# Performance work log

Measured on AMD Instinct MI355X. Metric: run time of the kernel, lower is better.

## Reference

```python
import jax, jax.numpy as jnp
import numpy as np

B, N, DIM = 4, 2048, 1024
HEADS, DHEAD = 16, 64
INNER = HEADS * DHEAD  # 1024


def _sigma(t):
    # elu(x) + 1 feature map (strictly positive)
    return jax.nn.elu(t) + 1.0


def setup_inputs() -> dict:
    key = jax.random.key(0)
    k1, k2, k3, k4, k5 = jax.random.split(key, 5)
    x = jax.random.normal(k1, (B, N, DIM), dtype=jnp.float32)
    M = jax.random.normal(k2, (B, HEADS, DHEAD, DHEAD), dtype=jnp.float32)
    Z = jnp.ones((B, HEADS, DHEAD, 1), dtype=jnp.float32)
    W_qkv = jax.random.normal(k3, (DIM, 3 * INNER), dtype=jnp.float32) * (DIM ** -0.5)
    beta_lin = jnp.ones((1,), dtype=jnp.float32) * 4.6     # Linear_Attention.beta
    beta_gate = jax.random.normal(k4, (1, HEADS, 1, 1), dtype=jnp.float32)  # per-head gate
    return {"x": x, "M": M, "Z": Z, "W_qkv": W_qkv, "beta_lin": beta_lin, "beta_gate": beta_gate}


def reference(x, M, Z, W_qkv, beta_lin, beta_gate):
    b, n, _ = x.shape
    scale = DHEAD ** -0.5

    qkv = x @ W_qkv                                   # [b, n, 3*inner]
    q, k, v = jnp.split(qkv, 3, axis=-1)
    # b n (h d) -> b h n d
    to_heads = lambda t: t.reshape(b, n, HEADS, DHEAD).transpose(0, 2, 1, 3)
    q, k, v = to_heads(q), to_heads(k), to_heads(v)

    # ---- linear-attention compressive memory branch ----
    sq = _sigma(q)                                    # [b h n d]
    sk = _sigma(k)
    A_mem = jnp.einsum('bhnd,bhdv->bhnv', sq, M) / jnp.einsum('bhnd,bhdi->bhni', sq, Z)
    moment = jnp.einsum('bhnd,bhdv->bhnv', sk, M) / jnp.einsum('bhnd,bhdi->bhni', sk, Z)

    # EMA state update (training path)
    beta_m = jnp.clip(jax.nn.sigmoid(beta_lin), 0.9, 0.999)  # scalar in (0.9, 0.999)
    Z_new = beta_m * Z + jnp.sum(sk, axis=-2)[..., None]      # [b h d 1]
    M_new = beta_m * M + jnp.einsum('bhnd,bhnv->bhdv', sk, v - moment)

    # ---- standard dot-product attention branch ----
    dots = jnp.einsum('bhid,bhjd->bhij', q, k) * scale
    attn = jax.nn.softmax(dots, axis=-1)
    A_dot = jnp.einsum('bhij,bhjd->bhid', attn, v)

    # ---- learned per-head gate ----
    g = jax.nn.sigmoid(beta_gate)                     # [1 h 1 1]
    A = g * A_mem + (1.0 - g) * A_dot                 # [b h n d]
    A = A.transpose(0, 2, 1, 3).reshape(b, n, INNER)  # b h n d -> b n (h d)
    return (A, M_new, Z_new)
```

## Files before the change

### kernel.cpp

```cpp
#include <hip/hip_runtime.h>
#include <math.h>

#define B_ 4
#define N_ 2048
#define DIM_ 1024
#define H_ 16
#define D_ 64
#define INNER_ 1024
#define BH_ (B_*H_)

#define A_ELEMS  (B_*N_*INNER_)
#define M_ELEMS  (BH_*D_*D_)
#define Z_ELEMS  (BH_*D_)

#define SC_LOG2E 0.18033688011112042f

typedef __attribute__((ext_vector_type(8))) short short8;
typedef __attribute__((ext_vector_type(4))) float f32x4;
typedef __attribute__((ext_vector_type(4))) unsigned short us4;
typedef unsigned short u16;

typedef const unsigned int __attribute__((address_space(1))) gu32;
typedef unsigned int __attribute__((address_space(3))) su32;

__device__ __forceinline__ u16 f2bf(float f) {
    unsigned int u = __float_as_uint(f);
    u += 0x7fffu + ((u >> 16) & 1u);
    return (u16)(u >> 16);
}
__device__ __forceinline__ float bf2f(u16 s) {
    return __uint_as_float(((unsigned int)s) << 16);
}
__device__ __forceinline__ float sigma_f(float x) {
    return x > 0.f ? x + 1.f : __expf(x);
}
__device__ __forceinline__ short8 sig8(short8 in) {
    short8 out;
    u16* ip = (u16*)&in; u16* op = (u16*)&out;
    #pragma unroll
    for (int c = 0; c < 8; c++) op[c] = f2bf(sigma_f(bf2f(ip[c])));
    return out;
}

__global__ __launch_bounds__(256) void cvt_x(const float* __restrict__ x,
                                             u16* __restrict__ xb) {
    long i = ((long)blockIdx.x * 256 + threadIdx.x) * 4;
    float4 f = *(const float4*)&x[i];
    us4 o = {f2bf(f.x), f2bf(f.y), f2bf(f.z), f2bf(f.w)};
    *(us4*)&xb[i] = o;
}

__global__ __launch_bounds__(256) void cvt_w(const float* __restrict__ W,
                                             u16* __restrict__ Wt) {
    __shared__ u16 T[64 * 68];
    const int t  = threadIdx.x;
    const int n0 = blockIdx.x * 64, k0 = blockIdx.y * 64;
    #pragma unroll
    for (int i = 0; i < 4; i++) {
        int r  = (t >> 4) + i * 16;
        int c4 = (t & 15) * 4;
        float4 f = *(const float4*)&W[(long)(k0 + r) * 3072 + n0 + c4];
        T[(c4 + 0) * 68 + r] = f2bf(f.x);
        T[(c4 + 1) * 68 + r] = f2bf(f.y);
        T[(c4 + 2) * 68 + r] = f2bf(f.z);
        T[(c4 + 3) * 68 + r] = f2bf(f.w);
    }
    __syncthreads();
    #pragma unroll
    for (int i = 0; i < 4; i++) {
        int n  = (t >> 4) + i * 16;
        int k4 = (t & 15) * 4;
        us4 o;
        o.x = T[n * 68 + k4];     o.y = T[n * 68 + k4 + 1];
        o.z = T[n * 68 + k4 + 2]; o.w = T[n * 68 + k4 + 3];
        *(us4*)&Wt[(long)(n0 + n) * 1024 + k0 + k4] = o;
    }
}

__global__ __launch_bounds__(256) void qkv_mfma(
    const u16* __restrict__ xb, const u16* __restrict__ Wt,
    u16* __restrict__ q, u16* __restrict__ k, u16* __restrict__ v) {
    __shared__ u16 As[2][128 * 32];
    __shared__ u16 Bs[2][128 * 32];
    const int t = threadIdx.x, w = t >> 6, lane = t & 63;
    const int quad = lane >> 4, l16 = lane & 15;

    const int lin = blockIdx.x;
    const int wg  = (lin & 7) * 192 + (lin >> 3);
    const int j0  = (wg % 24) * 128;
    const int m0  = (wg / 24) * 128;
    const int mw = (w >> 1) * 64, nw = (w & 1) * 64;

    const int srow = t >> 2;
    const int scol = (t & 3) * 8;

    const u16* pa0 = xb + (long)(m0 + srow) * 1024 + scol;
    const u16* pa1 = pa0 + (long)64 * 1024;
    const u16* pb0 = Wt + (long)(j0 + srow) * 1024 + scol;
    const u16* pb1 = pb0 + (long)64 * 1024;
    su32* da0 = (su32*)&As[0][srow * 32 + scol];
    su32* da1 = (su32*)&As[0][(srow + 64) * 32 + scol];
    su32* db0 = (su32*)&Bs[0][srow * 32 + scol];
    su32* db1 = (su32*)&Bs[0][(srow + 64) * 32 + scol];
    const int half = 128 * 32 / 2;

    f32x4 acc[4][4] = {};

    __builtin_amdgcn_global_load_lds((gu32*)pa0, da0, 16, 0, 0);
    __builtin_amdgcn_global_load_lds((gu32*)pa1, da1, 16, 0, 0);
    __builtin_amdgcn_global_load_lds((gu32*)pb0, db0, 16, 0, 0);
    __builtin_amdgcn_global_load_lds((gu32*)pb1, db1, 16, 0, 0);
    pa0 += 32; pa1 += 32; pb0 += 32; pb1 += 32;
    __syncthreads();

    for (int kt = 0; kt < 32; ++kt) {
        const int cur = kt & 1;
        if (kt + 1 < 32) {
            const int nxs = (cur ^ 1) * half;
            __builtin_amdgcn_global_load_lds((gu32*)pa0, da0 + nxs, 16, 0, 0);
            __builtin_amdgcn_global_load_lds((gu32*)pa1, da1 + nxs, 16, 0, 0);
            __builtin_amdgcn_global_load_lds((gu32*)pb0, db0 + nxs, 16, 0, 0);
            __builtin_amdgcn_global_load_lds((gu32*)pb1, db1 + nxs, 16, 0, 0);
            pa0 += 32; pa1 += 32; pb0 += 32; pb1 += 32;
        }

        short8 af[4], bf[4];
        #pragma unroll
        for (int mt = 0; mt < 4; mt++)
            af[mt] = *(const short8*)&As[cur][(mw + mt * 16 + l16) * 32 + quad * 8];
        #pragma unroll
        for (int nt = 0; nt < 4; nt++)
            bf[nt] = *(const short8*)&Bs[cur][(nw + nt * 16 + l16) * 32 + quad * 8];
        #pragma unroll
        for (int mt = 0; mt < 4; mt++)
            #pragma unroll
            for (int nt = 0; nt < 4; nt++)
                acc[mt][nt] = __builtin_amdgcn_mfma_f32_16x16x32_bf16(
                    af[mt], bf[nt], acc[mt][nt], 0, 0, 0);

        __syncthreads();
    }

    const int cb0 = j0 + nw;
    const int which = cb0 >> 10;
    u16* dstsel = (which == 0) ? q : (which == 1) ? k : v;
    const int bq = (m0 + mw) >> 11;
    const int nb = (m0 + mw) & 2047;
    const int lanoff = quad * 256 + l16;
    #pragma unroll
    for (int nt = 0; nt < 4; nt++) {
        const int cb = cb0 + nt * 16;
        const int hh = (cb & 1023) >> 6;
        const int dc = cb & 63;
        u16* dstp = dstsel + ((long)(bq * H_ + hh) * N_ + nb) * D_ + dc;
        #pragma unroll
        for (int mt = 0; mt < 4; mt++)
            #pragma unroll
            for (int r = 0; r < 4; r++)
                dstp[(mt * 16 + r) * 64 + lanoff] = f2bf(acc[mt][nt][r]);
    }
}

__global__ __launch_bounds__(256) void vt_transpose(
    const u16* __restrict__ vb, u16* __restrict__ vT) {
    __shared__ u16 T[64 * 72];
    const int bh = blockIdx.y;
    const int n0 = blockIdx.x * 64;
    const int t  = threadIdx.x;
    const int jj = t >> 3, kg = (t & 7) * 8;
    #pragma unroll
    for (int i = 0; i < 2; i++) {
        int j = jj + i * 32;
        short8 vv = *(const short8*)&vb[(((long)bh * N_ + n0 + j) << 6) + kg];
        u16* vp = (u16*)&vv;
        int jc = j ^ kg;
        #pragma unroll
        for (int c = 0; c < 8; c++) T[(kg + c) * 72 + jc] = vp[c];
    }
    __syncthreads();
    const int d = t >> 2, sg = (t & 3) * 16, xr = d & 56;
    short8 a0 = *(const short8*)&T[d * 72 + (sg ^ xr)];
    short8 a1 = *(const short8*)&T[d * 72 + ((sg + 8) ^ xr)];
    u16* dst = vT + ((long)bh * 64 + d) * 2048 + n0 + sg;
    *(short8*)dst       = a0;
    *(short8*)(dst + 8) = a1;
}

__global__ __launch_bounds__(256) void init_mz(
    const float* __restrict__ M, const float* __restrict__ Z,
    const float* __restrict__ beta_lin,
    float* __restrict__ outM, float* __restrict__ outZ) {
    float beta = 1.f / (1.f + __expf(-beta_lin[0]));
    beta = fminf(fmaxf(beta, 0.9f), 0.999f);
    int i = blockIdx.x * 256 + threadIdx.x;
    if (i < M_ELEMS) outM[i] = beta * M[i];
    if (i < Z_ELEMS) outZ[i] = beta * Z[i];
}

__global__ __launch_bounds__(256) void linear_mfma(
    const u16* __restrict__ qg, const u16* __restrict__ kg_,
    const u16* __restrict__ vTg, const float* __restrict__ Mg,
    const float* __restrict__ Zg, const float* __restrict__ beta_gate,
    float* __restrict__ outA, float* __restrict__ outM, float* __restrict__ outZ) {
    __shared__ u16 MTz[80 * 72];
    __shared__ u16 sqsh[64 * 72];
    __shared__ u16 sksh[64 * 72];
    __shared__ u16 skT[64 * 72];
    __shared__ u16 vT[64 * 72];
    __shared__ u16 vmT[80 * 72];
    __shared__ float dks[64];

    const int bh = blockIdx.y, b = bh >> 4, h = bh & 15;
    const int t = threadIdx.x, w = t >> 6, lane = t & 63;
    const int quad = lane >> 4, l16 = lane & 15;
    const long bhN = (long)bh * N_;

    #pragma unroll
    for (int i = 0; i < 4; i++) {
        int d  = (t >> 4) + i * 16;
        int c4 = (t & 15) * 4;
        float4 f = *(const float4*)&Mg[bh * 4096 + d * 64 + c4];
        MTz[(c4 + 0) * 72 + d] = f2bf(f.x);
        MTz[(c4 + 1) * 72 + d] = f2bf(f.y);
        MTz[(c4 + 2) * 72 + d] = f2bf(f.z);
        MTz[(c4 + 3) * 72 + d] = f2bf(f.w);
    }
    if (t < 64) {
        MTz[64 * 72 + t] = f2bf(Zg[bh * 64 + t]);
        vmT[64 * 72 + t] = f2bf(1.0f);
    }
    for (int e = t; e < 15 * 72; e += 256) {
        MTz[65 * 72 + e] = 0;
        vmT[65 * 72 + e] = 0;
    }
    if (t >= 64 && t < 72) { MTz[64 * 72 + t] = 0; vmT[64 * 72 + t] = 0; }

    const float g = 1.f / (1.f + __expf(-beta_gate[h]));

    f32x4 macc[5] = {};

    const int jj = t >> 3;
    const int kgp = (t & 7) * 8;
    const int srow = t >> 2;
    const int sg   = (t & 3) * 16;

    for (int c0 = 0; c0 < 256; c0 += 64) {
        const int n0c = blockIdx.x * 256 + c0;
        __syncthreads();

        #pragma unroll
        for (int i = 0; i < 2; i++) {
            int j = jj + i * 32;
            long gb = ((bhN + n0c + j) << 6) + kgp;
            short8 q8 = sig8(*(const short8*)&qg[gb]);
            short8 k8 = sig8(*(const short8*)&kg_[gb]);
            *(short8*)&sqsh[j * 72 + kgp] = q8;
            *(short8*)&sksh[j * 72 + kgp] = k8;
            u16* kp = (u16*)&k8;
            int jc = j ^ kgp;
            #pragma unroll
            for (int c = 0; c < 8; c++) skT[(kgp + c) * 72 + jc] = kp[c];
        }
        {
            const u16* vp = vTg + ((long)bh * 64 + srow) * 2048 + n0c + sg;
            *(short8*)&vT[srow * 72 + sg]     = *(const short8*)vp;
            *(short8*)&vT[srow * 72 + sg + 8] = *(const short8*)(vp + 8);
        }
        __syncthreads();

        {
            short8 a0 = *(const short8*)&sqsh[(w * 16 + l16) * 72 + quad * 8];
            short8 a1 = *(const short8*)&sqsh[(w * 16 + l16) * 72 + 32 + quad * 8];
            f32x4 am[5];
            #pragma unroll
            for (int ct = 0; ct < 5; ct++) {
                short8 b0 = *(const short8*)&MTz[(ct * 16 + l16) * 72 + quad * 8];
                short8 b1 = *(const short8*)&MTz[(ct * 16 + l16) * 72 + 32 + quad * 8];
                f32x4 acc = {};
                acc = __builtin_amdgcn_mfma_f32_16x16x32_bf16(a0, b0, acc, 0, 0, 0);
                acc = __builtin_amdgcn_mfma_f32_16x16x32_bf16(a1, b1, acc, 0, 0, 0);
                am[ct] = acc;
            }
            #pragma unroll
            for (int r = 0; r < 4; r++) {
                float dq  = __shfl(am[4][r], lane & 48, 64);
                float inv = __builtin_amdgcn_rcpf(dq);
                int n = n0c + w * 16 + quad * 4 + r;
                long row = ((long)(b * N_ + n)) * INNER_ + h * 64;
                #pragma unroll
                for (int ct = 0; ct < 4; ct++)
                    outA[row + ct * 16 + l16] = g * am[ct][r] * inv;
            }
        }

        f32x4 mt_[4];
        {
            short8 a0 = *(const short8*)&MTz[(w * 16 + l16) * 72 + quad * 8];
            short8 a1 = *(const short8*)&MTz[(w * 16 + l16) * 72 + 32 + quad * 8];
            #pragma unroll
            for (int ct = 0; ct < 4; ct++) {
                short8 b0 = *(const short8*)&sksh[(ct * 16 + l16) * 72 + quad * 8];
                short8 b1 = *(const short8*)&sksh[(ct * 16 + l16) * 72 + 32 + quad * 8];
                f32x4 acc = {};
                acc = __builtin_amdgcn_mfma_f32_16x16x32_bf16(a0, b0, acc, 0, 0, 0);
                acc = __builtin_amdgcn_mfma_f32_16x16x32_bf16(a1, b1, acc, 0, 0, 0);
                mt_[ct] = acc;
            }
            short8 z0 = *(const short8*)&MTz[(64 + l16) * 72 + quad * 8];
            short8 z1 = *(const short8*)&MTz[(64 + l16) * 72 + 32 + quad * 8];
            short8 b0 = *(const short8*)&sksh[(w * 16 + l16) * 72 + quad * 8];
            short8 b1 = *(const short8*)&sksh[(w * 16 + l16) * 72 + 32 + quad * 8];
            f32x4 acc = {};
            acc = __builtin_amdgcn_mfma_f32_16x16x32_bf16(z0, b0, acc, 0, 0, 0);
            acc = __builtin_amdgcn_mfma_f32_16x16x32_bf16(z1, b1, acc, 0, 0, 0);
            if (quad == 0) dks[w * 16 + l16] = __builtin_amdgcn_rcpf(acc[0]);
        }
        __syncthreads();

        #pragma unroll
        for (int ct = 0; ct < 4; ct++) {
            float invdk = dks[ct * 16 + l16];
            #pragma unroll
            for (int r = 0; r < 4; r++) {
                int vd = w * 16 + quad * 4 + r;
                float vv = bf2f(vT[vd * 72 + ct * 16 + l16]);
                vmT[vd * 72 + ct * 16 + l16] = f2bf(vv - mt_[ct][r] * invdk);
            }
        }
        __syncthreads();

        {
            int drow = w * 16 + l16, xr = drow & 56;
            short8 a0 = *(const short8*)&skT[drow * 72 + ((quad * 8) ^ xr)];
            short8 a1 = *(const short8*)&skT[drow * 72 + ((32 + quad * 8) ^ xr)];
            #pragma unroll
            for (int ct = 0; ct < 5; ct++) {
                short8 b0 = *(const short8*)&vmT[(ct * 16 + l16) * 72 + quad * 8];
                short8 b1 = *(const short8*)&vmT[(ct * 16 + l16) * 72 + 32 + quad * 8];
                macc[ct] = __builtin_amdgcn_mfma_f32_16x16x32_bf16(a0, b0, macc[ct], 0, 0, 0);
                macc[ct] = __builtin_amdgcn_mfma_f32_16x16x32_bf16(a1, b1, macc[ct], 0, 0, 0);
            }
        }
    }

    #pragma unroll
    for (int ct = 0; ct < 4; ct++)
        #pragma unroll
        for (int r = 0; r < 4; r++) {
            int d = w * 16 + quad * 4 + r;
            atomicAdd(&outM[bh * 4096 + d * 64 + ct * 16 + l16], macc[ct][r]);
        }
    if (l16 == 0)
        #pragma unroll
        for (int r = 0; r < 4; r++)
            atomicAdd(&outZ[bh * 64 + w * 16 + quad * 4 + r], macc[4][r]);
}

__global__ __launch_bounds__(256, 2) void flash_mfma(
    const u16* __restrict__ qb, const u16* __restrict__ kb,
    const u16* __restrict__ vTg, const float* __restrict__ beta_gate,
    float* __restrict__ outA) {
    __shared__ u16 Ks[64 * 68];
    __shared__ u16 Vt[64 * 68];

    const int lin = blockIdx.x;
    const int wg  = (lin & 7) * 64 + (lin >> 3);
    const int bh  = wg >> 3;
    const int n0  = (wg & 7) * 256;
    const int b = bh >> 4, h = bh & 15;
    const int t = threadIdx.x, w = t >> 6, lane = t & 63;
    const int quad = lane >> 4, l16 = lane & 15;
    const long bhN = (long)bh * N_;

    const int srow = t >> 2;
    const int sg   = (t & 3) * 16;
    const int jloc = srow & 31;
    const int krow = (srow & 32) + ((jloc & 4) << 2) + ((jloc >> 3) << 2) + (jloc & 3);

    const u16* kbase  = kb + (bhN << 6);
    const u16* vtbase = vTg + (long)bh * 64 * 2048;

    short8 qf[4][2];
    #pragma unroll
    for (int mi = 0; mi < 4; mi++) {
        long qrow = bhN + n0 + w * 64 + mi * 16 + l16;
        qf[mi][0] = *(const short8*)&qb[(qrow << 6) + quad * 8];
        qf[mi][1] = *(const short8*)&qb[(qrow << 6) + 32 + quad * 8];
        #pragma unroll
        for (int z = 0; z < 2; z++) {
            u16* p = (u16*)&qf[mi][z];
            #pragma unroll
            for (int c = 0; c < 8; c++) p[c] = f2bf(bf2f(p[c]) * SC_LOG2E);
        }
    }

    const short8 onesf = {0x3F80, 0x3F80, 0x3F80, 0x3F80,
                          0x3F80, 0x3F80, 0x3F80, 0x3F80};

    short8 kr0, kr1, vr0, vr1;
    {
        const u16* kp = kbase + ((long)srow << 6) + sg;
        kr0 = *(const short8*)kp;
        kr1 = *(const short8*)(kp + 8);
        const u16* vp = vtbase + (long)srow * 2048 + sg;
        vr0 = *(const short8*)vp;
        vr1 = *(const short8*)(vp + 8);
    }

    f32x4 of[4][4] = {};
    f32x4 ol[4] = {};

    for (int j0 = 0; j0 < N_; j0 += 64) {
        __syncthreads();
        *(short8*)&Ks[krow * 68 + sg]     = kr0;
        *(short8*)&Ks[krow * 68 + sg + 8] = kr1;
        *(short8*)&Vt[srow * 68 + sg]     = vr0;
        *(short8*)&Vt[srow * 68 + sg + 8] = vr1;
        __syncthreads();

        if (j0 + 64 < N_) {
            const u16* kp = kbase + ((long)(j0 + 64 + srow) << 6) + sg;
            kr0 = *(const short8*)kp;
            kr1 = *(const short8*)(kp + 8);
            const u16* vp = vtbase + (long)srow * 2048 + j0 + 64 + sg;
            vr0 = *(const short8*)vp;
            vr1 = *(const short8*)(vp + 8);
        }

        #pragma unroll
        for (int g = 0; g < 2; g++) {
            const int rb = g * 32;
            short8 kA0 = *(const short8*)&Ks[(rb + l16) * 68 + quad * 8];
            short8 kA1 = *(const short8*)&Ks[(rb + l16) * 68 + 32 + quad * 8];
            short8 kB0 = *(const short8*)&Ks[(rb + 16 + l16) * 68 + quad * 8];
            short8 kB1 = *(const short8*)&Ks[(rb + 16 + l16) * 68 + 32 + quad * 8];
            short8 vf[4];
            #pragma unroll
            for (int nt = 0; nt < 4; nt++)
                vf[nt] = *(const short8*)&Vt[(nt * 16 + l16) * 68 + rb + quad * 8];

            #pragma unroll
            for (int mi = 0; mi < 4; mi++) {
                f32x4 st0 = {}, st1 = {};
                __builtin_amdgcn_s_setprio(1);
                st0 = __builtin_amdgcn_mfma_f32_16x16x32_bf16(kA0, qf[mi][0], st0, 0, 0, 0);
                st0 = __builtin_amdgcn_mfma_f32_16x16x32_bf16(kA1, qf[mi][1], st0, 0, 0, 0);
                st1 = __builtin_amdgcn_mfma_f32_16x16x32_bf16(kB0, qf[mi][0], st1, 0, 0, 0);
                st1 = __builtin_amdgcn_mfma_f32_16x16x32_bf16(kB1, qf[mi][1], st1, 0, 0, 0);
                __builtin_amdgcn_s_setprio(0);
                float p0 = __builtin_amdgcn_exp2f(st0[0]);
                float p1 = __builtin_amdgcn_exp2f(st0[1]);
                float p2 = __builtin_amdgcn_exp2f(st0[2]);
                float p3 = __builtin_amdgcn_exp2f(st0[3]);
                float p4 = __builtin_amdgcn_exp2f(st1[0]);
                float p5 = __builtin_amdgcn_exp2f(st1[1]);
                float p6 = __builtin_amdgcn_exp2f(st1[2]);
                float p7 = __builtin_amdgcn_exp2f(st1[3]);
                short8 af;
                unsigned int* au = (unsigned int*)&af;
                au[0] = __builtin_amdgcn_perm(__float_as_uint(p1), __float_as_uint(p0),
                                              0x07060302u);
                au[1] = __builtin_amdgcn_perm(__float_as_uint(p3), __float_as_uint(p2),
                                              0x07060302u);
                au[2] = __builtin_amdgcn_perm(__float_as_uint(p5), __float_as_uint(p4),
                                              0x07060302u);
                au[3] = __builtin_amdgcn_perm(__float_as_uint(p7), __float_as_uint(p6),
                                              0x07060302u);
                __builtin_amdgcn_s_setprio(1);
                ol[mi] = __builtin_amdgcn_mfma_f32_16x16x32_bf16(af, onesf, ol[mi], 0, 0, 0);
                #pragma unroll
                for (int nt = 0; nt < 4; nt++)
                    of[mi][nt] = __builtin_amdgcn_mfma_f32_16x16x32_bf16(
                        af, vf[nt], of[mi][nt], 0, 0, 0);
                __builtin_amdgcn_s_setprio(0);
            }
        }
    }

    const float g  = 1.f / (1.f + __expf(-beta_gate[h]));
    const float gi = 1.f - g;
    #pragma unroll
    for (int mi = 0; mi < 4; mi++) {
        #pragma unroll
        for (int r = 0; r < 4; r++) {
            float sc = gi / ol[mi][r];
            int n = n0 + w * 64 + mi * 16 + quad * 4 + r;
            #pragma unroll
            for (int nt = 0; nt < 4; nt++) {
                long idx = ((long)(b * N_ + n)) * INNER_ + h * 64 + nt * 16 + l16;
                outA[idx] += sc * of[mi][nt][r];
            }
        }
    }
}

extern "C" void kernel_launch(void* const* d_in, const int* in_sizes, int n_in,
                              void* d_out, int out_size, void* d_ws, size_t ws_size,
                              hipStream_t stream) {
    const float* x         = (const float*)d_in[0];
    const float* M         = (const float*)d_in[1];
    const float* Z         = (const float*)d_in[2];
    const float* W         = (const float*)d_in[3];
    const float* beta_lin  = (const float*)d_in[4];
    const float* beta_gate = (const float*)d_in[5];

    float* out  = (float*)d_out;
    float* outA = out;
    float* outM = out + A_ELEMS;
    float* outZ = out + A_ELEMS + M_ELEMS;

    u16* xb = (u16*)d_ws;
    u16* Wt = xb + (size_t)8192 * 1024;
    u16* qb = Wt + (size_t)3072 * 1024;
    u16* kb = qb + (size_t)BH_ * N_ * D_;
    u16* vb = kb + (size_t)BH_ * N_ * D_;
    u16* vt = vb + (size_t)BH_ * N_ * D_;

    cvt_x<<<dim3(A_ELEMS / 1024), 256, 0, stream>>>(x, xb);
    cvt_w<<<dim3(48, 16), 256, 0, stream>>>(W, Wt);
    qkv_mfma<<<dim3(1536), 256, 0, stream>>>(xb, Wt, qb, kb, vb);
    vt_transpose<<<dim3(N_ / 64, BH_), 256, 0, stream>>>(vb, vt);
    init_mz<<<dim3((M_ELEMS + 255) / 256), 256, 0, stream>>>(M, Z, beta_lin, outM, outZ);
    linear_mfma<<<dim3(8, BH_), 256, 0, stream>>>(qb, kb, vt, M, Z, beta_gate,
                                                  outA, outM, outZ);
    flash_mfma<<<dim3(N_ / 256 * BH_), 256, 0, stream>>>(qb, kb, vt, beta_gate, outA);
}
```

Measured before the change: 268.9 us.

## Merge linear-memory and flash attention into one concurrently scheduled kernel

Combines the linear-attention memory kernel and the flash-attention kernel into a single launch of 1024 blocks. Each block picks its branch from its block index, interleaved per XCD, so both branches run at the same time instead of one after the other. Because the two branches now race on the output A, it is zeroed in init_mz and both branches accumulate into it with atomicAdd. This trades extra atomics, a full zeroing pass over A, and higher shared-memory use per block (which may cut flash occupancy, and launch bounds no longer request 2 blocks) for removing the serialization and tail of two back-to-back launches.

```diff
diff --git a/kernel.cpp b/kernel.cpp
--- a/kernel.cpp
+++ b/kernel.cpp
@@ -189,308 +189,313 @@
 __global__ __launch_bounds__(256) void init_mz(
     const float* __restrict__ M, const float* __restrict__ Z,
     const float* __restrict__ beta_lin,
-    float* __restrict__ outM, float* __restrict__ outZ) {
+    float* __restrict__ outM, float* __restrict__ outZ,
+    float* __restrict__ outA) {
     float beta = 1.f / (1.f + __expf(-beta_lin[0]));
     beta = fminf(fmaxf(beta, 0.9f), 0.999f);
     int i = blockIdx.x * 256 + threadIdx.x;
+    float4 z4 = {0.f, 0.f, 0.f, 0.f};
+    *(float4*)&outA[(long)i * 4] = z4;
     if (i < M_ELEMS) outM[i] = beta * M[i];
     if (i < Z_ELEMS) outZ[i] = beta * Z[i];
 }
 
-__global__ __launch_bounds__(256) void linear_mfma(
+__global__ __launch_bounds__(256) void fused_attn(
     const u16* __restrict__ qg, const u16* __restrict__ kg_,
     const u16* __restrict__ vTg, const float* __restrict__ Mg,
     const float* __restrict__ Zg, const float* __restrict__ beta_gate,
     float* __restrict__ outA, float* __restrict__ outM, float* __restrict__ outZ) {
+    __shared__ u16 Ks[64 * 68];
+    __shared__ u16 Vt[64 * 68];
     __shared__ u16 MTz[80 * 72];
     __shared__ u16 sqsh[64 * 72];
     __shared__ u16 sksh[64 * 72];
     __shared__ u16 skT[64 * 72];
-    __shared__ u16 vT[64 * 72];
+    __shared__ u16 vTl[64 * 72];
     __shared__ u16 vmT[80 * 72];
     __shared__ float dks[64];
 
-    const int bh = blockIdx.y, b = bh >> 4, h = bh & 15;
+    const int lin  = blockIdx.x;
+    const int xcd  = lin & 7;
+    const int gidx = lin >> 3;
+    const int sel  = gidx & 1;
+    const int u    = gidx >> 1;
+    const int idx  = xcd * 64 + u;
+
     const int t = threadIdx.x, w = t >> 6, lane = t & 63;
     const int quad = lane >> 4, l16 = lane & 15;
-    const long bhN = (long)bh * N_;
-
-    #pragma unroll
-    for (int i = 0; i < 4; i++) {
-        int d  = (t >> 4) + i * 16;
-        int c4 = (t & 15) * 4;
-        float4 f = *(const float4*)&Mg[bh * 4096 + d * 64 + c4];
-        MTz[(c4 + 0) * 72 + d] = f2bf(f.x);
-        MTz[(c4 + 1) * 72 + d] = f2bf(f.y);
-        MTz[(c4 + 2) * 72 + d] = f2bf(f.z);
-        MTz[(c4 + 3) * 72 + d] = f2bf(f.w);
-    }
-    if (t < 64) {
-        MTz[64 * 72 + t] = f2bf(Zg[bh * 64 + t]);
-        vmT[64 * 72 + t] = f2bf(1.0f);
-    }
-    for (int e = t; e < 15 * 72; e += 256) {
-        MTz[65 * 72 + e] = 0;
-        vmT[65 * 72 + e] = 0;
-    }
-    if (t >= 64 && t < 72) { MTz[64 * 72 + t] = 0; vmT[64 * 72 + t] = 0; }
-
-    const float g = 1.f / (1.f + __expf(-beta_gate[h]));
-
-    f32x4 macc[5] = {};
-
-    const int jj = t >> 3;
-    const int kgp = (t & 7) * 8;
-    const int srow = t >> 2;
-    const int sg   = (t & 3) * 16;
-
-    for (int c0 = 0; c0 < 256; c0 += 64) {
-        const int n0c = blockIdx.x * 256 + c0;
-        __syncthreads();
-
-        #pragma unroll
-        for (int i = 0; i < 2; i++) {
-            int j = jj + i * 32;
-            long gb = ((bhN + n0c + j) << 6) + kgp;
-            short8 q8 = sig8(*(const short8*)&qg[gb]);
-            short8 k8 = sig8(*(const short8*)&kg_[gb]);
-            *(short8*)&sqsh[j * 72 + kgp] = q8;
-            *(short8*)&sksh[j * 72 + kgp] = k8;
-            u16* kp = (u16*)&k8;
-            int jc = j ^ kgp;
-            #pragma unroll
-            for (int c = 0; c < 8; c++) skT[(kgp + c) * 72 + jc] = kp[c];
-        }
+
+    if (sel == 0) {
+        const int bh  = idx >> 3;
+        const int n0  = (idx & 7) * 256;
+        const int b = bh >> 4, h = bh & 15;
+        const long bhN = (long)bh * N_;
+
+        const int srow = t >> 2;
+        const int sg   = (t & 3) * 16;
+        const int jloc = srow & 31;
+        const int krow = (srow & 32) + ((jloc & 4) << 2) + ((jloc >> 3) << 2) + (jloc & 3);
+
+        const u16* kbase  = kg_ + (bhN << 6);
+        const u16* vtbase = vTg + (long)bh * 64 * 2048;
+
+        short8 qf[4][2];
+        #pragma unroll
+        for (int mi = 0; mi < 4; mi++) {
+            long qrow = bhN + n0 + w * 64 + mi * 16 + l16;
+            qf[mi][0] = *(const short8*)&qg[(qrow << 6) + quad * 8];
+            qf[mi][1] = *(const short8*)&qg[(qrow << 6) + 32 + quad * 8];
+            #pragma unroll
+            for (int z = 0; z < 2; z++) {
+                u16* p = (u16*)&qf[mi][z];
+                #pragma unroll
+                for (int c = 0; c < 8; c++) p[c] = f2bf(bf2f(p[c]) * SC_LOG2E);
+            }
+        }
+
+        const short8 onesf = {0x3F80, 0x3F80, 0x3F80, 0x3F80,
+                              0x3F80, 0x3F80, 0x3F80, 0x3F80};
+
+        short8 kr0, kr1, vr0, vr1;
         {
-            const u16* vp = vTg + ((long)bh * 64 + srow) * 2048 + n0c + sg;
-            *(short8*)&vT[srow * 72 + sg]     = *(const short8*)vp;
-            *(short8*)&vT[srow * 72 + sg + 8] = *(const short8*)(vp + 8);
-        }
-        __syncthreads();
-
-        {
-            short8 a0 = *(const short8*)&sqsh[(w * 16 + l16) * 72 + quad * 8];
-            short8 a1 = *(const short8*)&sqsh[(w * 16 + l16) * 72 + 32 + quad * 8];
-            f32x4 am[5];
-            #pragma unroll
-            for (int ct = 0; ct < 5; ct++) {
-                short8 b0 = *(const short8*)&MTz[(ct * 16 + l16) * 72 + quad * 8];
-                short8 b1 = *(const short8*)&MTz[(ct * 16 + l16) * 72 + 32 + quad * 8];
-                f32x4 acc = {};
-                acc = __builtin_amdgcn_mfma_f32_16x16x32_bf16(a0, b0, acc, 0, 0, 0);
-                acc = __builtin_amdgcn_mfma_f32_16x16x32_bf16(a1, b1, acc, 0, 0, 0);
-                am[ct] = acc;
-            }
-            #pragma unroll
-            for (int r = 0; r < 4; r++) {
-                float dq  = __shfl(am[4][r], lane & 48, 64);
-                float inv = __builtin_amdgcn_rcpf(dq);
-                int n = n0c + w * 16 + quad * 4 + r;
-                long row = ((long)(b * N_ + n)) * INNER_ + h * 64;
-                #pragma unroll
-                for (int ct = 0; ct < 4; ct++)
-                    outA[row + ct * 16 + l16] = g * am[ct][r] * inv;
-            }
-        }
-
-        f32x4 mt_[4];
-        {
-            short8 a0 = *(const short8*)&MTz[(w * 16 + l16) * 72 + quad * 8];
-            short8 a1 = *(const short8*)&MTz[(w * 16 + l16) * 72 + 32 + quad * 8];
-            #pragma unroll
-            for (int ct = 0; ct < 4; ct++) {
-                short8 b0 = *(const short8*)&sksh[(ct * 16 + l16) * 72 + quad * 8];
-                short8 b1 = *(const short8*)&sksh[(ct * 16 + l16) * 72 + 32 + quad * 8];
-                f32x4 acc = {};
-                acc = __builtin_amdgcn_mfma_f32_16x16x32_bf16(a0, b0, acc, 0, 0, 0);
-                acc = __builtin_amdgcn_mfma_f32_16x16x32_bf16(a1, b1, acc, 0, 0, 0);
-                mt_[ct] = acc;
-            }
-            short8 z0 = *(const short8*)&MTz[(64 + l16) * 72 + quad * 8];
-            short8 z1 = *(const short8*)&MTz[(64 + l16) * 72 + 32 + quad * 8];
-            short8 b0 = *(const short8*)&sksh[(w * 16 + l16) * 72 + quad * 8];
-            short8 b1 = *(const short8*)&sksh[(w * 16 + l16) * 72 + 32 + quad * 8];
-            f32x4 acc = {};
-            acc = __builtin_amdgcn_mfma_f32_16x16x32_bf16(z0, b0, acc, 0, 0, 0);
-            acc = __builtin_amdgcn_mfma_f32_16x16x32_bf16(z1, b1, acc, 0, 0, 0);
-            if (quad == 0) dks[w * 16 + l16] = __builtin_amdgcn_rcpf(acc[0]);
-        }
-        __syncthreads();
-
-        #pragma unroll
-        for (int ct = 0; ct < 4; ct++) {
-            float invdk = dks[ct * 16 + l16];
-            #pragma unroll
-            for (int r = 0; r < 4; r++) {
-                int vd = w * 16 + quad * 4 + r;
-                float vv = bf2f(vT[vd * 72 + ct * 16 + l16]);
-                vmT[vd * 72 + ct * 16 + l16] = f2bf(vv - mt_[ct][r] * invdk);
-            }
-        }
-        __syncthreads();
-
-        {
-            int drow = w * 16 + l16, xr = drow & 56;
-            short8 a0 = *(const short8*)&skT[drow * 72 + ((quad * 8) ^ xr)];
-            short8 a1 = *(const short8*)&skT[drow * 72 + ((32 + quad * 8) ^ xr)];
-            #pragma unroll
-            for (int ct = 0; ct < 5; ct++) {
-                short8 b0 = *(const short8*)&vmT[(ct * 16 + l16) * 72 + quad * 8];
-                short8 b1 = *(const short8*)&vmT[(ct * 16 + l16) * 72 + 32 + quad * 8];
-                macc[ct] = __builtin_amdgcn_mfma_f32_16x16x32_bf16(a0, b0, macc[ct], 0, 0, 0);
-                macc[ct] = __builtin_amdgcn_mfma_f32_16x16x32_bf16(a1, b1, macc[ct], 0, 0, 0);
-            }
-        }
-    }
-
-    #pragma unroll
-    for (int ct = 0; ct < 4; ct++)
-        #pragma unroll
-        for (int r = 0; r < 4; r++) {
-            int d = w * 16 + quad * 4 + r;
-            atomicAdd(&outM[bh * 4096 + d * 64 + ct * 16 + l16], macc[ct][r]);
-        }
-    if (l16 == 0)
-        #pragma unroll
-        for (int r = 0; r < 4; r++)
-            atomicAdd(&outZ[bh * 64 + w * 16 + quad * 4 + r], macc[4][r]);
-}
-
-__global__ __launch_bounds__(256, 2) void flash_mfma(
-    const u16* __restrict__ qb, const u16* __restrict__ kb,
-    const u16* __restrict__ vTg, const float* __restrict__ beta_gate,
-    float* __restrict__ outA) {
-    __shared__ u16 Ks[64 * 68];
-    __shared__ u16 Vt[64 * 68];
-
-    const int lin = blockIdx.x;
-    const int wg  = (lin & 7) * 64 + (lin >> 3);
-    const int bh  = wg >> 3;
-    const int n0  = (wg & 7) * 256;
-    const int b = bh >> 4, h = bh & 15;
-    const int t = threadIdx.x, w = t >> 6, lane = t & 63;
-    const int quad = lane >> 4, l16 = lane & 15;
-    const long bhN = (long)bh * N_;
-
-    const int srow = t >> 2;
-    const int sg   = (t & 3) * 16;
-    const int jloc = srow & 31;
-    const int krow = (srow & 32) + ((jloc & 4) << 2) + ((jloc >> 3) << 2) + (jloc & 3);
-
-    const u16* kbase  = kb + (bhN << 6);
-    const u16* vtbase = vTg + (long)bh * 64 * 2048;
-
-    short8 qf[4][2];
-    #pragma unroll
-    for (int mi = 0; mi < 4; mi++) {
-        long qrow = bhN + n0 + w * 64 + mi * 16 + l16;
-        qf[mi][0] = *(const short8*)&qb[(qrow << 6) + quad * 8];
-        qf[mi][1] = *(const short8*)&qb[(qrow << 6) + 32 + quad * 8];
-        #pragma unroll
-        for (int z = 0; z < 2; z++) {
-            u16* p = (u16*)&qf[mi][z];
-            #pragma unroll
-            for (int c = 0; c < 8; c++) p[c] = f2bf(bf2f(p[c]) * SC_LOG2E);
-        }
-    }
-
-    const short8 onesf = {0x3F80, 0x3F80, 0x3F80, 0x3F80,
-                          0x3F80, 0x3F80, 0x3F80, 0x3F80};
-
-    short8 kr0, kr1, vr0, vr1;
-    {
-        const u16* kp = kbase + ((long)srow << 6) + sg;
-        kr0 = *(const short8*)kp;
-        kr1 = *(const short8*)(kp + 8);
-        const u16* vp = vtbase + (long)srow * 2048 + sg;
-        vr0 = *(const short8*)vp;
-        vr1 = *(const short8*)(vp + 8);
-    }
-
-    f32x4 of[4][4] = {};
-    f32x4 ol[4] = {};
-
-    for (int j0 = 0; j0 < N_; j0 += 64) {
-        __syncthreads();
-        *(short8*)&Ks[krow * 68 + sg]     = kr0;
-        *(short8*)&Ks[krow * 68 + sg + 8] = kr1;
-        *(short8*)&Vt[srow * 68 + sg]     = vr0;
-        *(short8*)&Vt[srow * 68 + sg + 8] = vr1;
-        __syncthreads();
-
-        if (j0 + 64 < N_) {
-            const u16* kp = kbase + ((long)(j0 + 64 + srow) << 6) + sg;
+            const u16* kp = kbase + ((long)srow << 6) + sg;
             kr0 = *(const short8*)kp;
             kr1 = *(const short8*)(kp + 8);
-            const u16* vp = vtbase + (long)srow * 2048 + j0 + 64 + sg;
+            const u16* vp = vtbase + (long)srow * 2048 + sg;
             vr0 = *(const short8*)vp;
             vr1 = *(const short8*)(vp + 8);
         }
 
-        #pragma unroll
-        for (int g = 0; g < 2; g++) {
-            const int rb = g * 32;
-            short8 kA0 = *(const short8*)&Ks[(rb + l16) * 68 + quad * 8];
-            short8 kA1 = *(const short8*)&Ks[(rb + l16) * 68 + 32 + quad * 8];
-            short8 kB0 = *(const short8*)&Ks[(rb + 16 + l16) * 68 + quad * 8];
-            short8 kB1 = *(const short8*)&Ks[(rb + 16 + l16) * 68 + 32 + quad * 8];
-            short8 vf[4];
-            #pragma unroll
-            for (int nt = 0; nt < 4; nt++)
-                vf[nt] = *(const short8*)&Vt[(nt * 16 + l16) * 68 + rb + quad * 8];
-
-            #pragma unroll
-            for (int mi = 0; mi < 4; mi++) {
-                f32x4 st0 = {}, st1 = {};
-                __builtin_amdgcn_s_setprio(1);
-                st0 = __builtin_amdgcn_mfma_f32_16x16x32_bf16(kA0, qf[mi][0], st0, 0, 0, 0);
-                st0 = __builtin_amdgcn_mfma_f32_16x16x32_bf16(kA1, qf[mi][1], st0, 0, 0, 0);
-                st1 = __builtin_amdgcn_mfma_f32_16x16x32_bf16(kB0, qf[mi][0], st1, 0, 0, 0);
-                st1 = __builtin_amdgcn_mfma_f32_16x16x32_bf16(kB1, qf[mi][1], st1, 0, 0, 0);
-                __builtin_amdgcn_s_setprio(0);
-                float p0 = __builtin_amdgcn_exp2f(st0[0]);
-                float p1 = __builtin_amdgcn_exp2f(st0[1]);
-                float p2 = __builtin_amdgcn_exp2f(st0[2]);
-                float p3 = __builtin_amdgcn_exp2f(st0[3]);
-                float p4 = __builtin_amdgcn_exp2f(st1[0]);
-                float p5 = __builtin_amdgcn_exp2f(st1[1]);
-                float p6 = __builtin_amdgcn_exp2f(st1[2]);
-                float p7 = __builtin_amdgcn_exp2f(st1[3]);
-                short8 af;
-                unsigned int* au = (unsigned int*)&af;
-                au[0] = __builtin_amdgcn_perm(__float_as_uint(p1), __float_as_uint(p0),
-                                              0x07060302u);
-                au[1] = __builtin_amdgcn_perm(__float_as_uint(p3), __float_as_uint(p2),
-                                              0x07060302u);
-                au[2] = __builtin_amdgcn_perm(__float_as_uint(p5), __float_as_uint(p4),
-                                              0x07060302u);
-                au[3] = __builtin_amdgcn_perm(__float_as_uint(p7), __float_as_uint(p6),
-                                              0x07060302u);
-                __builtin_amdgcn_s_setprio(1);
-                ol[mi] = __builtin_amdgcn_mfma_f32_16x16x32_bf16(af, onesf, ol[mi], 0, 0, 0);
+        f32x4 of[4][4] = {};
+        f32x4 ol[4] = {};
+
+        for (int j0 = 0; j0 < N_; j0 += 64) {
+            __syncthreads();
+            *(short8*)&Ks[krow * 68 + sg]     = kr0;
+            *(short8*)&Ks[krow * 68 + sg + 8] = kr1;
+            *(short8*)&Vt[srow * 68 + sg]     = vr0;
+            *(short8*)&Vt[srow * 68 + sg + 8] = vr1;
+            __syncthreads();
+
+            if (j0 + 64 < N_) {
+                const u16* kp = kbase + ((long)(j0 + 64 + srow) << 6) + sg;
+                kr0 = *(const short8*)kp;
+                kr1 = *(const short8*)(kp + 8);
+                const u16* vp = vtbase + (long)srow * 2048 + j0 + 64 + sg;
+                vr0 = *(const short8*)vp;
+                vr1 = *(const short8*)(vp + 8);
+            }
+
+            #pragma unroll
+            for (int g2 = 0; g2 < 2; g2++) {
+                const int rb = g2 * 32;
+                short8 kA0 = *(const short8*)&Ks[(rb + l16) * 68 + quad * 8];
+                short8 kA1 = *(const short8*)&Ks[(rb + l16) * 68 + 32 + quad * 8];
+                short8 kB0 = *(const short8*)&Ks[(rb + 16 + l16) * 68 + quad * 8];
+                short8 kB1 = *(const short8*)&Ks[(rb + 16 + l16) * 68 + 32 + quad * 8];
+                short8 vf[4];
                 #pragma unroll
                 for (int nt = 0; nt < 4; nt++)
-                    of[mi][nt] = __builtin_amdgcn_mfma_f32_16x16x32_bf16(
-                        af, vf[nt], of[mi][nt], 0, 0, 0);
-                __builtin_amdgcn_s_setprio(0);
-            }
-        }
-    }
-
-    const float g  = 1.f / (1.f + __expf(-beta_gate[h]));
-    const float gi = 1.f - g;
-    #pragma unroll
-    for (int mi = 0; mi < 4; mi++) {
-        #pragma unroll
-        for (int r = 0; r < 4; r++) {
-            float sc = gi / ol[mi][r];
-            int n = n0 + w * 64 + mi * 16 + quad * 4 + r;
-            #pragma unroll
-            for (int nt = 0; nt < 4; nt++) {
-                long idx = ((long)(b * N_ + n)) * INNER_ + h * 64 + nt * 16 + l16;
-                outA[idx] += sc * of[mi][nt][r];
-            }
-        }
+                    vf[nt] = *(const short8*)&Vt[(nt * 16 + l16) * 68 + rb + quad * 8];
+
+                #pragma unroll
+                for (int mi = 0; mi < 4; mi++) {
+                    f32x4 st0 = {}, st1 = {};
+                    __builtin_amdgcn_s_setprio(1);
+                    st0 = __builtin_amdgcn_mfma_f32_16x16x32_bf16(kA0, qf[mi][0], st0, 0, 0, 0);
+                    st0 = __builtin_amdgcn_mfma_f32_16x16x32_bf16(kA1, qf[mi][1], st0, 0, 0, 0);
+                    st1 = __builtin_amdgcn_mfma_f32_16x16x32_bf16(kB0, qf[mi][0], st1, 0, 0, 0);
+                    st1 = __builtin_amdgcn_mfma_f32_16x16x32_bf16(kB1, qf[mi][1], st1, 0, 0, 0);
+                    __builtin_amdgcn_s_setprio(0);
+                    float p0 = __builtin_amdgcn_exp2f(st0[0]);
+                    float p1 = __builtin_amdgcn_exp2f(st0[1]);
+                    float p2 = __builtin_amdgcn_exp2f(st0[2]);
+                    float p3 = __builtin_amdgcn_exp2f(st0[3]);
+                    float p4 = __builtin_amdgcn_exp2f(st1[0]);
+                    float p5 = __builtin_amdgcn_exp2f(st1[1]);
+                    float p6 = __builtin_amdgcn_exp2f(st1[2]);
+                    float p7 = __builtin_amdgcn_exp2f(st1[3]);
+                    short8 af;
+                    unsigned int* au = (unsigned int*)&af;
+                    au[0] = __builtin_amdgcn_perm(__float_as_uint(p1), __float_as_uint(p0),
+                                                  0x07060302u);
+                    au[1] = __builtin_amdgcn_perm(__float_as_uint(p3), __float_as_uint(p2),
+                                                  0x07060302u);
+                    au[2] = __builtin_amdgcn_perm(__float_as_uint(p5), __float_as_uint(p4),
+                                                  0x07060302u);
+                    au[3] = __builtin_amdgcn_perm(__float_as_uint(p7), __float_as_uint(p6),
+                                                  0x07060302u);
+                    __builtin_amdgcn_s_setprio(1);
+                    ol[mi] = __builtin_amdgcn_mfma_f32_16x16x32_bf16(af, onesf, ol[mi], 0, 0, 0);
+                    #pragma unroll
+                    for (int nt = 0; nt < 4; nt++)
+                        of[mi][nt] = __builtin_amdgcn_mfma_f32_16x16x32_bf16(
+                            af, vf[nt], of[mi][nt], 0, 0, 0);
+                    __builtin_amdgcn_s_setprio(0);
+                }
+            }
+        }
+
+        const float g  = 1.f / (1.f + __expf(-beta_gate[h]));
+        const float gi = 1.f - g;
+        #pragma unroll
+        for (int mi = 0; mi < 4; mi++) {
+            #pragma unroll
+            for (int r = 0; r < 4; r++) {
+                float sc = gi / ol[mi][r];
+                int n = n0 + w * 64 + mi * 16 + quad * 4 + r;
+                #pragma unroll
+                for (int nt = 0; nt < 4; nt++) {
+                    long idx2 = ((long)(b * N_ + n)) * INNER_ + h * 64 + nt * 16 + l16;
+                    atomicAdd(&outA[idx2], sc * of[mi][nt][r]);
+                }
+            }
+        }
+    } else {
+        const int bh = idx >> 3;
+        const int bx = idx & 7;
+        const int b = bh >> 4, h = bh & 15;
+        const long bhN = (long)bh * N_;
+
+        #pragma unroll
+        for (int i = 0; i < 4; i++) {
+            int d  = (t >> 4) + i * 16;
+            int c4 = (t & 15) * 4;
+            float4 f = *(const float4*)&Mg[bh * 4096 + d * 64 + c4];
+            MTz[(c4 + 0) * 72 + d] = f2bf(f.x);
+            MTz[(c4 + 1) * 72 + d] = f2bf(f.y);
+            MTz[(c4 + 2) * 72 + d] = f2bf(f.z);
+            MTz[(c4 + 3) * 72 + d] = f2bf(f.w);
+        }
+        if (t < 64) {
+            MTz[64 * 72 + t] = f2bf(Zg[bh * 64 + t]);
+            vmT[64 * 72 + t] = f2bf(1.0f);
+        }
+        for (int e = t; e < 15 * 72; e += 256) {
+            MTz[65 * 72 + e] = 0;
+            vmT[65 * 72 + e] = 0;
+        }
+        if (t >= 64 && t < 72) { MTz[64 * 72 + t] = 0; vmT[64 * 72 + t] = 0; }
+
+        const float g = 1.f / (1.f + __expf(-beta_gate[h]));
+
+        f32x4 macc[5] = {};
+
+        const int jj = t >> 3;
+        const int kgp = (t & 7) * 8;
+        const int srow = t >> 2;
+        const int sg   = (t & 3) * 16;
+
+        for (int c0 = 0; c0 < 256; c0 += 64) {
+            const int n0c = bx * 256 + c0;
+            __syncthreads();
+
+            #pragma unroll
+            for (int i = 0; i < 2; i++) {
+                int j = jj + i * 32;
+                long gb = ((bhN + n0c + j) << 6) + kgp;
+                short8 q8 = sig8(*(const short8*)&qg[gb]);
+                short8 k8 = sig8(*(const short8*)&kg_[gb]);
+                *(short8*)&sqsh[j * 72 + kgp] = q8;
+                *(short8*)&sksh[j * 72 + kgp] = k8;
+                u16* kp = (u16*)&k8;
+                int jc = j ^ kgp;
+                #pragma unroll
+                for (int c = 0; c < 8; c++) skT[(kgp + c) * 72 + jc] = kp[c];
+            }
+            {
+                const u16* vp = vTg + ((long)bh * 64 + srow) * 2048 + n0c + sg;
+                *(short8*)&vTl[srow * 72 + sg]     = *(const short8*)vp;
+                *(short8*)&vTl[srow * 72 + sg + 8] = *(const short8*)(vp + 8);
+            }
+            __syncthreads();
+
+            {
+                short8 a0 = *(const short8*)&sqsh[(w * 16 + l16) * 72 + quad * 8];
+                short8 a1 = *(const short8*)&sqsh[(w * 16 + l16) * 72 + 32 + quad * 8];
+                f32x4 am[5];
+                #pragma unroll
+                for (int ct = 0; ct < 5; ct++) {
+                    short8 b0 = *(const short8*)&MTz[(ct * 16 + l16) * 72 + quad * 8];
+                    short8 b1 = *(const short8*)&MTz[(ct * 16 + l16) * 72 + 32 + quad * 8];
+                    f32x4 acc = {};
+                    acc = __builtin_amdgcn_mfma_f32_16x16x32_bf16(a0, b0, acc, 0, 0, 0);
+                    acc = __builtin_amdgcn_mfma_f32_16x16x32_bf16(a1, b1, acc, 0, 0, 0);
+                    am[ct] = acc;
+                }
+                #pragma unroll
+                for (int r = 0; r < 4; r++) {
+                    float dq  = __shfl(am[4][r], lane & 48, 64);
+                    float inv = __builtin_amdgcn_rcpf(dq);
+                    int n = n0c + w * 16 + quad * 4 + r;
+                    long row = ((long)(b * N_ + n)) * INNER_ + h * 64;
+                    #pragma unroll
+                    for (int ct = 0; ct < 4; ct++)
+                        atomicAdd(&outA[row + ct * 16 + l16], g * am[ct][r] * inv);
+                }
+            }
+
+            f32x4 mt_[4];
+            {
+                short8 a0 = *(const short8*)&MTz[(w * 16 + l16) * 72 + quad * 8];
+                short8 a1 = *(const short8*)&MTz[(w * 16 + l16) * 72 + 32 + quad * 8];
+                #pragma unroll
+                for (int ct = 0; ct < 4; ct++) {
+                    short8 b0 = *(const short8*)&sksh[(ct * 16 + l16) * 72 + quad * 8];
+                    short8 b1 = *(const short8*)&sksh[(ct * 16 + l16) * 72 + 32 + quad * 8];
+                    f32x4 acc = {};
+                    acc = __builtin_amdgcn_mfma_f32_16x16x32_bf16(a0, b0, acc, 0, 0, 0);
+                    acc = __builtin_amdgcn_mfma_f32_16x16x32_bf16(a1, b1, acc, 0, 0, 0);
+                    mt_[ct] = acc;
+                }
+                short8 z0 = *(const short8*)&MTz[(64 + l16) * 72 + quad * 8];
+                short8 z1 = *(const short8*)&MTz[(64 + l16) * 72 + 32 + quad * 8];
+                short8 b0 = *(const short8*)&sksh[(w * 16 + l16) * 72 + quad * 8];
+                short8 b1 = *(const short8*)&sksh[(w * 16 + l16) * 72 + 32 + quad * 8];
+                f32x4 acc = {};
+                acc = __builtin_amdgcn_mfma_f32_16x16x32_bf16(z0, b0, acc, 0, 0, 0);
+                acc = __builtin_amdgcn_mfma_f32_16x16x32_bf16(z1, b1, acc, 0, 0, 0);
+                if (quad == 0) dks[w * 16 + l16] = __builtin_amdgcn_rcpf(acc[0]);
+            }
+            __syncthreads();
+
+            #pragma unroll
+            for (int ct = 0; ct < 4; ct++) {
+                float invdk = dks[ct * 16 + l16];
+                #pragma unroll
+                for (int r = 0; r < 4; r++) {
+                    int vd = w * 16 + quad * 4 + r;
+                    float vv = bf2f(vTl[vd * 72 + ct * 16 + l16]);
+                    vmT[vd * 72 + ct * 16 + l16] = f2bf(vv - mt_[ct][r] * invdk);
+                }
+            }
+            __syncthreads();
+
+            {
+                int drow = w * 16 + l16, xr = drow & 56;
+                short8 a0 = *(const short8*)&skT[drow * 72 + ((quad * 8) ^ xr)];
+                short8 a1 = *(const short8*)&skT[drow * 72 + ((32 + quad * 8) ^ xr)];
+                #pragma unroll
+                for (int ct = 0; ct < 5; ct++) {
+                    short8 b0 = *(const short8*)&vmT[(ct * 16 + l16) * 72 + quad * 8];
+                    short8 b1 = *(const short8*)&vmT[(ct * 16 + l16) * 72 + 32 + quad * 8];
+                    macc[ct] = __builtin_amdgcn_mfma_f32_16x16x32_bf16(a0, b0, macc[ct], 0, 0, 0);
+                    macc[ct] = __builtin_amdgcn_mfma_f32_16x16x32_bf16(a1, b1, macc[ct], 0, 0, 0);
+                }
+            }
+        }
+
+        #pragma unroll
+        for (int ct = 0; ct < 4; ct++)
+            #pragma unroll
+            for (int r = 0; r < 4; r++) {
+                int d = w * 16 + quad * 4 + r;
+                atomicAdd(&outM[bh * 4096 + d * 64 + ct * 16 + l16], macc[ct][r]);
+            }
+        if (l16 == 0)
+            #pragma unroll
+            for (int r = 0; r < 4; r++)
+                atomicAdd(&outZ[bh * 64 + w * 16 + quad * 4 + r], macc[4][r]);
     }
 }
 
@@ -520,8 +525,7 @@
     cvt_w<<<dim3(48, 16), 256, 0, stream>>>(W, Wt);
     qkv_mfma<<<dim3(1536), 256, 0, stream>>>(xb, Wt, qb, kb, vb);
     vt_transpose<<<dim3(N_ / 64, BH_), 256, 0, stream>>>(vb, vt);
-    init_mz<<<dim3((M_ELEMS + 255) / 256), 256, 0, stream>>>(M, Z, beta_lin, outM, outZ);
-    linear_mfma<<<dim3(8, BH_), 256, 0, stream>>>(qb, kb, vt, M, Z, beta_gate,
-                                                  outA, outM, outZ);
-    flash_mfma<<<dim3(N_ / 256 * BH_), 256, 0, stream>>>(qb, kb, vt, beta_gate, outA);
-}
+    init_mz<<<dim3(A_ELEMS / 1024), 256, 0, stream>>>(M, Z, beta_lin, outM, outZ, outA);
+    fused_attn<<<dim3(1024), 256, 0, stream>>>(qb, kb, vt, M, Z, beta_gate,
+                                               outA, outM, outZ);
+}
```

Result: slower. 312.8 us (+16.3%).

## Triple-buffer QKV GEMM LDS tiles with partial vmcnt waits and single barrier

Applied to the files above, without the earlier changes.

Turns the QKV projection GEMM's double-buffered LDS pipeline into a three-stage ring. Two tiles are prefetched ahead, and each iteration waits only for the older load group (vmcnt(4)) before one barrier, replacing the full syncthreads wait. This is meant to hide global-to-LDS latency behind MFMA work. It uses more LDS per block, which could lower occupancy, and it relies on hand-placed waitcnt being correct.

```diff
diff --git a/kernel.cpp b/kernel.cpp
--- a/kernel.cpp
+++ b/kernel.cpp
@@ -80,8 +80,8 @@
 __global__ __launch_bounds__(256) void qkv_mfma(
     const u16* __restrict__ xb, const u16* __restrict__ Wt,
     u16* __restrict__ q, u16* __restrict__ k, u16* __restrict__ v) {
-    __shared__ u16 As[2][128 * 32];
-    __shared__ u16 Bs[2][128 * 32];
+    __shared__ u16 As[3][128 * 32];
+    __shared__ u16 Bs[3][128 * 32];
     const int t = threadIdx.x, w = t >> 6, lane = t & 63;
     const int quad = lane >> 4, l16 = lane & 15;
 
@@ -111,34 +111,62 @@
     __builtin_amdgcn_global_load_lds((gu32*)pb0, db0, 16, 0, 0);
     __builtin_amdgcn_global_load_lds((gu32*)pb1, db1, 16, 0, 0);
     pa0 += 32; pa1 += 32; pb0 += 32; pb1 += 32;
-    __syncthreads();
-
-    for (int kt = 0; kt < 32; ++kt) {
-        const int cur = kt & 1;
-        if (kt + 1 < 32) {
-            const int nxs = (cur ^ 1) * half;
-            __builtin_amdgcn_global_load_lds((gu32*)pa0, da0 + nxs, 16, 0, 0);
-            __builtin_amdgcn_global_load_lds((gu32*)pa1, da1 + nxs, 16, 0, 0);
-            __builtin_amdgcn_global_load_lds((gu32*)pb0, db0 + nxs, 16, 0, 0);
-            __builtin_amdgcn_global_load_lds((gu32*)pb1, db1 + nxs, 16, 0, 0);
+    {
+        const int o = half;
+        __builtin_amdgcn_global_load_lds((gu32*)pa0, da0 + o, 16, 0, 0);
+        __builtin_amdgcn_global_load_lds((gu32*)pa1, da1 + o, 16, 0, 0);
+        __builtin_amdgcn_global_load_lds((gu32*)pb0, db0 + o, 16, 0, 0);
+        __builtin_amdgcn_global_load_lds((gu32*)pb1, db1 + o, 16, 0, 0);
+        pa0 += 32; pa1 += 32; pb0 += 32; pb1 += 32;
+    }
+
+    #pragma unroll 1
+    for (int kt = 0; kt < 31; ++kt) {
+        asm volatile("s_waitcnt vmcnt(4)" ::: "memory");
+        __builtin_amdgcn_s_barrier();
+
+        if (kt + 2 < 32) {
+            const int o = ((kt + 2) % 3) * half;
+            __builtin_amdgcn_global_load_lds((gu32*)pa0, da0 + o, 16, 0, 0);
+            __builtin_amdgcn_global_load_lds((gu32*)pa1, da1 + o, 16, 0, 0);
+            __builtin_amdgcn_global_load_lds((gu32*)pb0, db0 + o, 16, 0, 0);
+            __builtin_amdgcn_global_load_lds((gu32*)pb1, db1 + o, 16, 0, 0);
             pa0 += 32; pa1 += 32; pb0 += 32; pb1 += 32;
         }
 
+        const int cs = (kt % 3) * (128 * 32);
         short8 af[4], bf[4];
         #pragma unroll
         for (int mt = 0; mt < 4; mt++)
-            af[mt] = *(const short8*)&As[cur][(mw + mt * 16 + l16) * 32 + quad * 8];
+            af[mt] = *(const short8*)&As[0][cs + (mw + mt * 16 + l16) * 32 + quad * 8];
         #pragma unroll
         for (int nt = 0; nt < 4; nt++)
-            bf[nt] = *(const short8*)&Bs[cur][(nw + nt * 16 + l16) * 32 + quad * 8];
+            bf[nt] = *(const short8*)&Bs[0][cs + (nw + nt * 16 + l16) * 32 + quad * 8];
         #pragma unroll
         for (int mt = 0; mt < 4; mt++)
             #pragma unroll
             for (int nt = 0; nt < 4; nt++)
                 acc[mt][nt] = __builtin_amdgcn_mfma_f32_16x16x32_bf16(
                     af[mt], bf[nt], acc[mt][nt], 0, 0, 0);
-
-        __syncthreads();
+    }
+
+    {
+        asm volatile("s_waitcnt vmcnt(0)" ::: "memory");
+        __builtin_amdgcn_s_barrier();
+        const int cs = (31 % 3) * (128 * 32);
+        short8 af[4], bf[4];
+        #pragma unroll
+        for (int mt = 0; mt < 4; mt++)
+            af[mt] = *(const short8*)&As[0][cs + (mw + mt * 16 + l16) * 32 + quad * 8];
+        #pragma unroll
+        for (int nt = 0; nt < 4; nt++)
+            bf[nt] = *(const short8*)&Bs[0][cs + (nw + nt * 16 + l16) * 32 + quad * 8];
+        #pragma unroll
+        for (int mt = 0; mt < 4; mt++)
+            #pragma unroll
+            for (int nt = 0; nt < 4; nt++)
+                acc[mt][nt] = __builtin_amdgcn_mfma_f32_16x16x32_bf16(
+                    af[mt], bf[nt], acc[mt][nt], 0, 0, 0);
     }
 
     const int cb0 = j0 + nw;
```

New measurement: 262.9 us. -2.2%, faster.
